# Kernel optimization log

Hardware: AMD Instinct MI355X
Metric: run time of the kernel (lower is better)

The kernel has to match this reference:

```python
import jax, jax.numpy as jnp
import numpy as np
from jax import lax

W = 50      # window size
EPS = 1e-5  # BatchNorm eps (torch default)


def setup_inputs() -> dict:
    key = jax.random.key(0)
    ks = jax.random.split(key, 40)
    def n(i, shape, s=0.1):
        return (jax.random.normal(ks[i], shape, dtype=jnp.float32) * s).astype(jnp.float32)
    inp = {}
    inp['x'] = jax.random.normal(ks[0], (16, 1, 2048), dtype=jnp.float32)
    # conv stack (eval-mode BatchNorm: running mean/var are params)
    inp['conv1_w'] = n(1, (64, 1, 9));  inp['conv1_b'] = n(2, (64,))
    inp['bn1_g'] = 1.0 + n(3, (64,));   inp['bn1_b'] = n(4, (64,))
    inp['bn1_m'] = n(5, (64,));         inp['bn1_v'] = 0.5 + jax.random.uniform(ks[6], (64,), dtype=jnp.float32)
    inp['conv2_w'] = n(7, (32, 64, 7)); inp['conv2_b'] = n(8, (32,))
    inp['bn2_g'] = 1.0 + n(9, (32,));   inp['bn2_b'] = n(10, (32,))
    inp['bn2_m'] = n(11, (32,));        inp['bn2_v'] = 0.5 + jax.random.uniform(ks[12], (32,), dtype=jnp.float32)
    inp['conv3_w'] = n(13, (16, 32, 5)); inp['conv3_b'] = n(14, (16,))
    inp['bn3_g'] = 1.0 + n(15, (16,));   inp['bn3_b'] = n(16, (16,))
    inp['bn3_m'] = n(17, (16,));         inp['bn3_v'] = 0.5 + jax.random.uniform(ks[18], (16,), dtype=jnp.float32)
    # 2-layer LSTM, hidden 64, input 16 (torch gate order i,f,g,o)
    H = 64
    inp['wih0'] = n(19, (4 * H, 16)); inp['whh0'] = n(20, (4 * H, H))
    inp['bih0'] = n(21, (4 * H,));    inp['bhh0'] = n(22, (4 * H,))
    inp['wih1'] = n(23, (4 * H, H));  inp['whh1'] = n(24, (4 * H, H))
    inp['bih1'] = n(25, (4 * H,));    inp['bhh1'] = n(26, (4 * H,))
    # classifier 64 -> 32 -> 2
    inp['fc1_w'] = n(27, (32, H)); inp['fc1_b'] = n(28, (32,))
    inp['fc2_w'] = n(29, (2, 32)); inp['fc2_b'] = n(30, (2,))
    return inp


def _conv1d(x, w, b, pad):
    # x: [N, Cin, L], w: [Cout, Cin, K]
    y = lax.conv_general_dilated(x, w, (1,), [(pad, pad)],
                                 dimension_numbers=('NCH', 'OIH', 'NCH'))
    return y + b[:, None]


def _bn(x, g, b, m, v):
    # eval-mode BatchNorm1d over channel dim of [N, C, L]
    return (x - m[:, None]) * (g / jnp.sqrt(v + EPS))[:, None] + b[:, None]


def _lstm_layer(x, wih, whh, bih, bhh):
    # x: [B, T, D] -> [B, T, H]; torch gate order (i, f, g, o)
    B, T, D = x.shape
    H = whh.shape[1]
    xs = jnp.transpose(x, (1, 0, 2))                     # [T, B, D]
    pre = xs @ wih.T + (bih + bhh)                       # [T, B, 4H] input projection, hoisted
    def step(carry, p):
        h, c = carry
        g = p + h @ whh.T
        i, f, gg, o = jnp.split(g, 4, axis=-1)
        c = jax.nn.sigmoid(f) * c + jax.nn.sigmoid(i) * jnp.tanh(gg)
        h = jax.nn.sigmoid(o) * jnp.tanh(c)
        return (h, c), h
    h0 = jnp.zeros((B, H), x.dtype)
    _, hs = lax.scan(step, (h0, h0), pre)
    return jnp.transpose(hs, (1, 0, 2))


def reference(x, conv1_w, conv1_b, bn1_g, bn1_b, bn1_m, bn1_v,
              conv2_w, conv2_b, bn2_g, bn2_b, bn2_m, bn2_v,
              conv3_w, conv3_b, bn3_g, bn3_b, bn3_m, bn3_v,
              wih0, whh0, bih0, bhh0, wih1, whh1, bih1, bhh1,
              fc1_w, fc1_b, fc2_w, fc2_b):
    B, C, T = x.shape
    # sliding windows with left zero-pad of W-1 -> [B, T, C, W]
    xp = jnp.pad(x, ((0, 0), (0, 0), (W - 1, 0)))
    idx = jnp.arange(T)[:, None] + jnp.arange(W)[None, :]  # [T, W]
    win = xp[:, :, idx]                                    # [B, C, T, W]
    win = jnp.transpose(win, (0, 2, 1, 3)).reshape(B * T, C, W)
    # conv -> BN(eval) -> ReLU stack (dropout is identity in eval)
    h = jax.nn.relu(_bn(_conv1d(win, conv1_w, conv1_b, 4), bn1_g, bn1_b, bn1_m, bn1_v))
    h = jax.nn.relu(_bn(_conv1d(h, conv2_w, conv2_b, 3), bn2_g, bn2_b, bn2_m, bn2_v))
    h = jax.nn.relu(_bn(_conv1d(h, conv3_w, conv3_b, 2), bn3_g, bn3_b, bn3_m, bn3_v))
    feats = h.mean(axis=-1).reshape(B, T, -1)              # AdaptiveAvgPool1d(1) -> [B, T, 16]
    # 2-layer LSTM
    h1 = _lstm_layer(feats, wih0, whh0, bih0, bhh0)
    h2 = _lstm_layer(h1, wih1, whh1, bih1, bhh1)           # [B, T, 64]
    # classifier
    z = jax.nn.relu(h2 @ fc1_w.T + fc1_b)
    logits = z @ fc2_w.T + fc2_b                           # [B, T, 2]
    return logits
```

## Files before the change

### kernel.cpp

```cpp
#include <hip/hip_runtime.h>

#define EPSV 1e-5f
#define SCOPE_AGENT __HIP_MEMORY_SCOPE_AGENT

__device__ __forceinline__ float fast_rcp(float x) { return __builtin_amdgcn_rcpf(x); }
__device__ __forceinline__ float tanhfast(float x) {
    float e = __expf(2.0f * x);
    return 1.0f - 2.0f * fast_rcp(e + 1.0f);
}
__device__ __forceinline__ float dot4(const float4 w, const float4 v, float a) {
    a = fmaf(w.x, v.x, a);
    a = fmaf(w.y, v.y, a);
    a = fmaf(w.z, v.z, a);
    a = fmaf(w.w, v.w, a);
    return a;
}
#define DPPF(v, ctrl) __int_as_float(__builtin_amdgcn_mov_dpp(__float_as_int(v), (ctrl), 0xF, 0xF, false))

typedef unsigned long long ull;

struct CnnS {
    float winh[64];
    float w1t[576];
    float a1[64 * 84 + 32];
    float a2[32 * 56 + 16];
    float s1[64], t1[64], s2[32], t2[32], s3[16], t3[16];
    float psum[256];
};
struct RecS {
    float hbuf[2][80];
    float ring[16][64];
    float xst[16][80];
};

__global__ void pack_kernel(const float* __restrict__ w2, const float* __restrict__ w3,
                            float* __restrict__ w2t2, float4* __restrict__ w3p4,
                            float* __restrict__ w3p1, int* __restrict__ sync_ints) {
    int j = blockIdx.x * 256 + threadIdx.x;
    if (j < 16384) {
        int i = j >> 8;
        int o = (j >> 3) & 31;
        int k = j & 7;
        w2t2[j] = (k < 7) ? w2[o * 448 + i * 7 + k] : 0.0f;
    } else if (j < 16896) {
        int e = j - 16384;
        int i = e >> 4, o = e & 15;
        int base = o * 160 + i * 5;
        w3p4[e] = make_float4(w3[base], w3[base + 1], w3[base + 2], w3[base + 3]);
        w3p1[e] = w3[base + 4];
    } else if (j < 16896 + 4096) {
        sync_ints[j - 16896] = 0;
    }
}

__device__ __forceinline__ void rec0_body(char* smemraw, int b,
    const float* __restrict__ feats,
    const float* __restrict__ wih, const float* __restrict__ whh,
    const float* __restrict__ bih, const float* __restrict__ bhh,
    float* __restrict__ hout, int* __restrict__ cnt0, int* __restrict__ flag1)
{
    RecS* s = (RecS*)smemraw;
    const int tid = threadIdx.x;
    const int j = tid >> 2, kq = tid & 3;

    const float4* pa = (const float4*)(whh + (0 * 64 + j) * 64 + kq * 16);
    const float4* pb = (const float4*)(whh + (1 * 64 + j) * 64 + kq * 16);
    const float4* pc_ = (const float4*)(whh + (2 * 64 + j) * 64 + kq * 16);
    const float4* pd = (const float4*)(whh + (3 * 64 + j) * 64 + kq * 16);
    float4 A0 = pa[0], A1 = pa[1], A2 = pa[2], A3 = pa[3];
    float4 B0 = pb[0], B1 = pb[1], B2 = pb[2], B3 = pb[3];
    float4 C0 = pc_[0], C1 = pc_[1], C2 = pc_[2], C3 = pc_[3];
    float4 D0 = pd[0], D1 = pd[1], D2 = pd[2], D3 = pd[3];
    float4 xw0 = *(const float4*)(wih + (0 * 64 + j) * 16 + kq * 4);
    float4 xw1 = *(const float4*)(wih + (1 * 64 + j) * 16 + kq * 4);
    float4 xw2 = *(const float4*)(wih + (2 * 64 + j) * 16 + kq * 4);
    float4 xw3 = *(const float4*)(wih + (3 * 64 + j) * 16 + kq * 4);
    const float bb0 = bih[j] + bhh[j];
    const float bb1 = bih[64 + j] + bhh[64 + j];
    const float bb2 = bih[128 + j] + bhh[128 + j];
    const float bb3 = bih[192 + j] + bhh[192 + j];

    if (tid < 64) s->hbuf[1][(tid >> 4) * 20 + (tid & 15)] = 0.0f;
    float cst = 0.0f;
    const float* fbase = feats + (long)b * 32768;
    __syncthreads();

#define STEP0(k) { \
        const float4* hp_ = (const float4*)&s->hbuf[((k) + 1) & 1][kq * 20]; \
        float4 h0_ = hp_[0], h1_ = hp_[1], h2_ = hp_[2], h3_ = hp_[3]; \
        float4 xv_ = *(const float4*)&s->xst[(k)][kq * 4]; \
        float p0 = dot4(A3, h3_, dot4(A2, h2_, dot4(A1, h1_, dot4(A0, h0_, dot4(xw0, xv_, 0.f))))); \
        float p1 = dot4(B3, h3_, dot4(B2, h2_, dot4(B1, h1_, dot4(B0, h0_, dot4(xw1, xv_, 0.f))))); \
        float p2 = dot4(C3, h3_, dot4(C2, h2_, dot4(C1, h1_, dot4(C0, h0_, dot4(xw2, xv_, 0.f))))); \
        float p3 = dot4(D3, h3_, dot4(D2, h2_, dot4(D1, h1_, dot4(D0, h0_, dot4(xw3, xv_, 0.f))))); \
        p0 += DPPF(p0, 0xB1); p1 += DPPF(p1, 0xB1); p2 += DPPF(p2, 0xB1); p3 += DPPF(p3, 0xB1); \
        p0 += DPPF(p0, 0x4E); p1 += DPPF(p1, 0x4E); p2 += DPPF(p2, 0x4E); p3 += DPPF(p3, 0x4E); \
        float gi = 1.0f - fast_rcp(__expf(p0 + bb0) + 1.0f); \
        float gf = 1.0f - fast_rcp(__expf(p1 + bb1) + 1.0f); \
        float gg = 1.0f - 2.0f * fast_rcp(__expf(2.0f * (p2 + bb2)) + 1.0f); \
        float go = 1.0f - fast_rcp(__expf(p3 + bb3) + 1.0f); \
        cst = fmaf(gf, cst, gi * gg); \
        float h_ = go * tanhfast(cst); \
        if (kq == 0) { s->hbuf[(k) & 1][(j >> 4) * 20 + (j & 15)] = h_; s->ring[(k)][j] = h_; } \
        __syncthreads(); \
    }

    for (int c = 0; c < 128; ++c) {
        if (tid == 0) {
            while (__hip_atomic_load(&cnt0[b * 128 + c], __ATOMIC_RELAXED, SCOPE_AGENT) < 16)
                __builtin_amdgcn_s_sleep(2);
        }
        __syncthreads();
        s->xst[tid >> 4][tid & 15] =
            __hip_atomic_load(fbase + c * 256 + tid, __ATOMIC_RELAXED, SCOPE_AGENT);
        __syncthreads();
        STEP0(0)  STEP0(1)  STEP0(2)  STEP0(3)
        STEP0(4)  STEP0(5)  STEP0(6)  STEP0(7)
        STEP0(8)  STEP0(9)  STEP0(10) STEP0(11)
        STEP0(12) STEP0(13) STEP0(14) STEP0(15)
        {
            ull* dst = (ull*)(hout + ((long)b * 2048 + c * 16) * 64);
            ull v0 = ((const ull*)s->ring)[tid];
            ull v1 = ((const ull*)s->ring)[tid + 256];
            __hip_atomic_store(dst + tid, v0, __ATOMIC_RELAXED, SCOPE_AGENT);
            __hip_atomic_store(dst + tid + 256, v1, __ATOMIC_RELAXED, SCOPE_AGENT);
            __syncthreads();
            if (tid == 0)
                __hip_atomic_store(&flag1[b * 128 + c], 1, __ATOMIC_RELAXED, SCOPE_AGENT);
        }
    }
#undef STEP0
}

__device__ __forceinline__ void rec1_body(char* smemraw, int b,
    const float* __restrict__ h1o,
    const float* __restrict__ wih, const float* __restrict__ whh,
    const float* __restrict__ bih, const float* __restrict__ bhh,
    float* __restrict__ hout, int* __restrict__ flag1)
{
    RecS* s = (RecS*)smemraw;
    const int tid = threadIdx.x;
    const int j = tid >> 2, kq = tid & 3;

    const float4* pa = (const float4*)(whh + (0 * 64 + j) * 64 + kq * 16);
    const float4* pb = (const float4*)(whh + (1 * 64 + j) * 64 + kq * 16);
    const float4* pc_ = (const float4*)(whh + (2 * 64 + j) * 64 + kq * 16);
    const float4* pd = (const float4*)(whh + (3 * 64 + j) * 64 + kq * 16);
    float4 A0 = pa[0], A1 = pa[1], A2 = pa[2], A3 = pa[3];
    float4 B0 = pb[0], B1 = pb[1], B2 = pb[2], B3 = pb[3];
    float4 C0 = pc_[0], C1 = pc_[1], C2 = pc_[2], C3 = pc_[3];
    float4 D0 = pd[0], D1 = pd[1], D2 = pd[2], D3 = pd[3];
    const float4* qa = (const float4*)(wih + (0 * 64 + j) * 64 + kq * 16);
    const float4* qb = (const float4*)(wih + (1 * 64 + j) * 64 + kq * 16);
    const float4* qc = (const float4*)(wih + (2 * 64 + j) * 64 + kq * 16);
    const float4* qd = (const float4*)(wih + (3 * 64 + j) * 64 + kq * 16);
    float4 XA0 = qa[0], XA1 = qa[1], XA2 = qa[2], XA3 = qa[3];
    float4 XB0 = qb[0], XB1 = qb[1], XB2 = qb[2], XB3 = qb[3];
    float4 XC0 = qc[0], XC1 = qc[1], XC2 = qc[2], XC3 = qc[3];
    float4 XD0 = qd[0], XD1 = qd[1], XD2 = qd[2], XD3 = qd[3];
    const float bb0 = bih[j] + bhh[j];
    const float bb1 = bih[64 + j] + bhh[64 + j];
    const float bb2 = bih[128 + j] + bhh[128 + j];
    const float bb3 = bih[192 + j] + bhh[192 + j];

    if (tid < 64) s->hbuf[1][(tid >> 4) * 20 + (tid & 15)] = 0.0f;
    float cst = 0.0f;
    __syncthreads();

#define STEP1(k) { \
        const float4* hp_ = (const float4*)&s->hbuf[((k) + 1) & 1][kq * 20]; \
        float4 h0_ = hp_[0], h1_ = hp_[1], h2_ = hp_[2], h3_ = hp_[3]; \
        const float4* xp_ = (const float4*)&s->xst[(k)][kq * 20]; \
        float4 x0_ = xp_[0], x1_ = xp_[1], x2_ = xp_[2], x3_ = xp_[3]; \
        float p0 = dot4(A3, h3_, dot4(A2, h2_, dot4(A1, h1_, dot4(A0, h0_, \
                   dot4(XA3, x3_, dot4(XA2, x2_, dot4(XA1, x1_, dot4(XA0, x0_, 0.f)))))))); \
        float p1 = dot4(B3, h3_, dot4(B2, h2_, dot4(B1, h1_, dot4(B0, h0_, \
                   dot4(XB3, x3_, dot4(XB2, x2_, dot4(XB1, x1_, dot4(XB0, x0_, 0.f)))))))); \
        float p2 = dot4(C3, h3_, dot4(C2, h2_, dot4(C1, h1_, dot4(C0, h0_, \
                   dot4(XC3, x3_, dot4(XC2, x2_, dot4(XC1, x1_, dot4(XC0, x0_, 0.f)))))))); \
        float p3 = dot4(D3, h3_, dot4(D2, h2_, dot4(D1, h1_, dot4(D0, h0_, \
                   dot4(XD3, x3_, dot4(XD2, x2_, dot4(XD1, x1_, dot4(XD0, x0_, 0.f)))))))); \
        p0 += DPPF(p0, 0xB1); p1 += DPPF(p1, 0xB1); p2 += DPPF(p2, 0xB1); p3 += DPPF(p3, 0xB1); \
        p0 += DPPF(p0, 0x4E); p1 += DPPF(p1, 0x4E); p2 += DPPF(p2, 0x4E); p3 += DPPF(p3, 0x4E); \
        float gi = 1.0f - fast_rcp(__expf(p0 + bb0) + 1.0f); \
        float gf = 1.0f - fast_rcp(__expf(p1 + bb1) + 1.0f); \
        float gg = 1.0f - 2.0f * fast_rcp(__expf(2.0f * (p2 + bb2)) + 1.0f); \
        float go = 1.0f - fast_rcp(__expf(p3 + bb3) + 1.0f); \
        cst = fmaf(gf, cst, gi * gg); \
        float h_ = go * tanhfast(cst); \
        if (kq == 0) { s->hbuf[(k) & 1][(j >> 4) * 20 + (j & 15)] = h_; s->ring[(k)][j] = h_; } \
        __syncthreads(); \
    }

    for (int c = 0; c < 128; ++c) {
        if (tid == 0) {
            while (__hip_atomic_load(&flag1[b * 128 + c], __ATOMIC_RELAXED, SCOPE_AGENT) < 1)
                __builtin_amdgcn_s_sleep(2);
        }
        __syncthreads();
        {
            const ull* src = (const ull*)(h1o + ((long)b * 2048 + c * 16) * 64);
            ull v0 = __hip_atomic_load(src + tid, __ATOMIC_RELAXED, SCOPE_AGENT);
            ull v1 = __hip_atomic_load(src + tid + 256, __ATOMIC_RELAXED, SCOPE_AGENT);
            int u0 = tid, u1 = tid + 256;
            int k0 = u0 >> 5, p0i = (u0 & 31) * 2;
            int k1 = u1 >> 5, p1i = (u1 & 31) * 2;
            *(ull*)&s->xst[k0][(p0i >> 4) * 20 + (p0i & 15)] = v0;
            *(ull*)&s->xst[k1][(p1i >> 4) * 20 + (p1i & 15)] = v1;
        }
        __syncthreads();
        STEP1(0)  STEP1(1)  STEP1(2)  STEP1(3)
        STEP1(4)  STEP1(5)  STEP1(6)  STEP1(7)
        STEP1(8)  STEP1(9)  STEP1(10) STEP1(11)
        STEP1(12) STEP1(13) STEP1(14) STEP1(15)
        {
            float4* dst = (float4*)(hout + ((long)b * 2048 + c * 16) * 64);
            dst[tid] = ((const float4*)s->ring)[tid];
        }
    }
#undef STEP1
}

__global__ __launch_bounds__(256, 2) void fused_kernel(
    const float* __restrict__ x,
    const float* __restrict__ w1, const float* __restrict__ b1,
    const float* __restrict__ g1, const float* __restrict__ be1,
    const float* __restrict__ m1, const float* __restrict__ v1,
    const float* __restrict__ b2,
    const float* __restrict__ g2, const float* __restrict__ be2,
    const float* __restrict__ m2, const float* __restrict__ v2,
    const float* __restrict__ b3,
    const float* __restrict__ g3, const float* __restrict__ be3,
    const float* __restrict__ m3, const float* __restrict__ v3,
    const float* __restrict__ w2t2,
    const float4* __restrict__ w3p4, const float* __restrict__ w3p1,
    const float* __restrict__ wih0, const float* __restrict__ whh0,
    const float* __restrict__ bih0, const float* __restrict__ bhh0,
    const float* __restrict__ wih1, const float* __restrict__ whh1,
    const float* __restrict__ bih1, const float* __restrict__ bhh1,
    float* __restrict__ feats, float* __restrict__ h1o, float* __restrict__ h2o,
    int* __restrict__ cnt0, int* __restrict__ flag1)
{
    __shared__ __align__(16) char smem[sizeof(CnnS)];
    static_assert(sizeof(RecS) <= sizeof(CnnS), "RecS must fit in CnnS");

    if (blockIdx.x < 16) { rec0_body(smem, blockIdx.x, feats, wih0, whh0, bih0, bhh0, h1o, cnt0, flag1); return; }
    if (blockIdx.x < 32) { rec1_body(smem, blockIdx.x - 16, h1o, wih1, whh1, bih1, bhh1, h2o, flag1); return; }

    CnnS* cs = (CnnS*)smem;
    const int tid = threadIdx.x;
    const int w = blockIdx.x - 32;
    const int b = w & 15;
    const int t = w >> 4;

    for (int idx = tid; idx < 576; idx += 256) {
        int o = idx / 9, k = idx % 9;
        cs->w1t[k * 64 + o] = w1[idx];
    }
    if (tid < 64) {
        float s = g1[tid] * rsqrtf(v1[tid] + EPSV);
        cs->s1[tid] = s;
        cs->t1[tid] = (b1[tid] - m1[tid]) * s + be1[tid];
    } else if (tid < 96) {
        int o = tid - 64;
        float s = g2[o] * rsqrtf(v2[o] + EPSV);
        cs->s2[o] = s;
        cs->t2[o] = (b2[o] - m2[o]) * s + be2[o];
    } else if (tid < 112) {
        int o = tid - 96;
        float s = g3[o] * rsqrtf(v3[o] + EPSV);
        cs->s3[o] = s;
        cs->t3[o] = (b3[o] - m3[o]) * s + be3[o];
    }
    if (tid < 64) {
        cs->winh[tid] = 0.0f;
        float* r = &cs->a1[tid * 84];
        r[0] = 0.f; r[1] = 0.f; r[2] = 0.f;
        r[77] = 0.f; r[78] = 0.f; r[79] = 0.f;
    }
    if (tid < 32) {
        float* r = &cs->a2[tid * 56];
        r[0] = 0.f; r[1] = 0.f;
        r[52] = 0.f; r[53] = 0.f; r[54] = 0.f; r[55] = 0.f;
    }
    __syncthreads();
    if (tid < 50) {
        int gi = t + tid - 49;
        cs->winh[4 + tid] = (gi >= 0) ? x[b * 2048 + gi] : 0.0f;
    }
    __syncthreads();

    {
        int o = tid >> 2, pg = tid & 3;
        int p0 = pg * 13;
        float wv[9];
        #pragma unroll
        for (int k = 0; k < 9; ++k) wv[k] = cs->w1t[k * 64 + o];
        float sc = cs->s1[o], tc = cs->t1[o];
        #pragma unroll
        for (int q = 0; q < 13; ++q) {
            int p = p0 + q;
            if (p < 50) {
                float acc = 0.0f;
                #pragma unroll
                for (int k = 0; k < 9; ++k) acc = fmaf(wv[k], cs->winh[p + k], acc);
                int pi = p + 3;
                int slot = pi + ((pi >> 3) << 2);
                cs->a1[o * 84 + slot] = fmaxf(acc * sc + tc, 0.0f);
            }
        }
    }
    __syncthreads();

    {
        int o = tid >> 3, pg = tid & 7;
        float acc[8];
        #pragma unroll
        for (int q = 0; q < 8; ++q) acc[q] = 0.0f;
        for (int i = 0; i < 64; ++i) {
            const float* rowp = &cs->a1[i * 84 + 12 * pg];
            float4 A0 = *(const float4*)&rowp[0];
            float4 A1 = *(const float4*)&rowp[4];
            float4 A2 = *(const float4*)&rowp[12];
            float2 A3 = *(const float2*)&rowp[16];
            const float4* wp = (const float4*)&w2t2[(i * 32 + o) * 8];
            float4 Wa = wp[0], Wb = wp[1];
            float av[14] = {A0.x, A0.y, A0.z, A0.w, A1.x, A1.y, A1.z, A1.w,
                            A2.x, A2.y, A2.z, A2.w, A3.x, A3.y};
            float wk[7] = {Wa.x, Wa.y, Wa.z, Wa.w, Wb.x, Wb.y, Wb.z};
            #pragma unroll
            for (int k = 0; k < 7; ++k) {
                #pragma unroll
                for (int q = 0; q < 8; ++q) acc[q] = fmaf(wk[k], av[q + k], acc[q]);
            }
        }
        float sc = cs->s2[o], tc = cs->t2[o];
        float r[8];
        #pragma unroll
        for (int q = 0; q < 8; ++q) r[q] = fmaxf(acc[q] * sc + tc, 0.0f);
        float* row = &cs->a2[o * 56 + 8 * pg];
        if (pg < 6) {
            *(float2*)&row[2] = make_float2(r[0], r[1]);
            *(float4*)&row[4] = make_float4(r[2], r[3], r[4], r[5]);
            *(float2*)&row[8] = make_float2(r[6], r[7]);
        } else if (pg == 6) {
            *(float2*)&row[2] = make_float2(r[0], r[1]);
        }
    }
    __syncthreads();

    {
        int o = tid & 15, pg = tid >> 4;
        float acc[4];
        #pragma unroll
        for (int q = 0; q < 4; ++q) acc[q] = 0.0f;
        for (int i = 0; i < 32; ++i) {
            float4 wa = w3p4[i * 16 + o];
            float w4 = w3p1[i * 16 + o];
            const float4* ap = (const float4*)&cs->a2[i * 56 + 4 * pg];
            float4 Aa = ap[0], Ab = ap[1];
            float av[8] = {Aa.x, Aa.y, Aa.z, Aa.w, Ab.x, Ab.y, Ab.z, Ab.w};
            #pragma unroll
            for (int q = 0; q < 4; ++q) {
                acc[q] = fmaf(wa.x, av[q], acc[q]);
                acc[q] = fmaf(wa.y, av[q + 1], acc[q]);
                acc[q] = fmaf(wa.z, av[q + 2], acc[q]);
                acc[q] = fmaf(wa.w, av[q + 3], acc[q]);
                acc[q] = fmaf(w4,   av[q + 4], acc[q]);
            }
        }
        float sc = cs->s3[o], tc = cs->t3[o];
        float ps = 0.0f;
        #pragma unroll
        for (int q = 0; q < 4; ++q) {
            int p = 4 * pg + q;
            if (p < 50) ps += fmaxf(acc[q] * sc + tc, 0.0f);
        }
        cs->psum[pg * 16 + o] = ps;
    }
    __syncthreads();

    if (tid < 16) {
        float s = 0.0f;
        #pragma unroll
        for (int pg = 0; pg < 16; ++pg) s += cs->psum[pg * 16 + tid];
        __hip_atomic_store(&feats[((long)b * 2048 + t) * 16 + tid], s * (1.0f / 50.0f),
                           __ATOMIC_RELAXED, SCOPE_AGENT);
    }
    __syncthreads();
    if (tid == 0)
        __hip_atomic_fetch_add(&cnt0[b * 128 + (t >> 4)], 1, __ATOMIC_RELAXED, SCOPE_AGENT);
}

__global__ __launch_bounds__(256) void fc_kernel(
    const float* __restrict__ h2o,
    const float* __restrict__ fc1w, const float* __restrict__ fc1b,
    const float* __restrict__ fc2w, const float* __restrict__ fc2b,
    float* __restrict__ out)
{
    int r = blockIdx.x * 256 + threadIdx.x;
    float h[64];
    const float4* hp = (const float4*)(h2o + (long)r * 64);
    #pragma unroll
    for (int i = 0; i < 16; ++i) {
        float4 v = hp[i];
        h[4 * i] = v.x; h[4 * i + 1] = v.y; h[4 * i + 2] = v.z; h[4 * i + 3] = v.w;
    }
    float l0 = fc2b[0], l1 = fc2b[1];
    #pragma unroll 4
    for (int j = 0; j < 32; ++j) {
        float z = fc1b[j];
        #pragma unroll
        for (int k = 0; k < 64; ++k) z = fmaf(h[k], fc1w[j * 64 + k], z);
        z = fmaxf(z, 0.0f);
        l0 = fmaf(z, fc2w[j], l0);
        l1 = fmaf(z, fc2w[32 + j], l1);
    }
    out[r * 2] = l0;
    out[r * 2 + 1] = l1;
}

extern "C" void kernel_launch(void* const* d_in, const int* in_sizes, int n_in,
                              void* d_out, int out_size, void* d_ws, size_t ws_size,
                              hipStream_t stream) {
    const float* x    = (const float*)d_in[0];
    const float* w1   = (const float*)d_in[1];
    const float* b1   = (const float*)d_in[2];
    const float* g1   = (const float*)d_in[3];
    const float* be1  = (const float*)d_in[4];
    const float* m1   = (const float*)d_in[5];
    const float* v1   = (const float*)d_in[6];
    const float* w2   = (const float*)d_in[7];
    const float* b2   = (const float*)d_in[8];
    const float* g2   = (const float*)d_in[9];
    const float* be2  = (const float*)d_in[10];
    const float* m2   = (const float*)d_in[11];
    const float* v2   = (const float*)d_in[12];
    const float* w3   = (const float*)d_in[13];
    const float* b3   = (const float*)d_in[14];
    const float* g3   = (const float*)d_in[15];
    const float* be3  = (const float*)d_in[16];
    const float* m3   = (const float*)d_in[17];
    const float* v3   = (const float*)d_in[18];
    const float* wih0 = (const float*)d_in[19];
    const float* whh0 = (const float*)d_in[20];
    const float* bih0 = (const float*)d_in[21];
    const float* bhh0 = (const float*)d_in[22];
    const float* wih1 = (const float*)d_in[23];
    const float* whh1 = (const float*)d_in[24];
    const float* bih1 = (const float*)d_in[25];
    const float* bhh1 = (const float*)d_in[26];
    const float* fc1w = (const float*)d_in[27];
    const float* fc1b = (const float*)d_in[28];
    const float* fc2w = (const float*)d_in[29];
    const float* fc2b = (const float*)d_in[30];
    float* out = (float*)d_out;

    float* ws    = (float*)d_ws;
    float* feats = ws;
    float* h2o   = feats + 32768 * 16;
    float* w2t2  = h2o + 32768 * 64;
    float* w3p4f = w2t2 + 16384;
    float* w3p1  = w3p4f + 2048;
    float* h1o   = w3p1 + 512;
    int*   cnt0  = (int*)(h1o + 32768 * 64);
    int*   flag1 = cnt0 + 2048;

    hipLaunchKernelGGL(pack_kernel, dim3(82), dim3(256), 0, stream,
                       w2, w3, w2t2, (float4*)w3p4f, w3p1, cnt0);
    hipLaunchKernelGGL(fused_kernel, dim3(32 + 32768), dim3(256), 0, stream,
                       x, w1, b1, g1, be1, m1, v1, b2, g2, be2, m2, v2,
                       b3, g3, be3, m3, v3, w2t2, (const float4*)w3p4f, w3p1,
                       wih0, whh0, bih0, bhh0, wih1, whh1, bih1, bhh1,
                       feats, h1o, h2o, cnt0, flag1);
    hipLaunchKernelGGL(fc_kernel, dim3(128), dim3(256), 0, stream,
                       h2o, fc1w, fc1b, fc2w, fc2b, out);
}
```

Before: 1.339 ms.

## Share interior conv outputs across overlapping windows; compute only edge positions per window

```diff
diff --git a/kernel.cpp b/kernel.cpp
--- a/kernel.cpp
+++ b/kernel.cpp
@@ -19,18 +19,18 @@
 
 typedef unsigned long long ull;
 
-struct CnnS {
-    float winh[64];
-    float w1t[576];
-    float a1[64 * 84 + 32];
-    float a2[32 * 56 + 16];
-    float s1[64], t1[64], s2[32], t2[32], s3[16], t3[16];
-    float psum[256];
-};
 struct RecS {
     float hbuf[2][80];
     float ring[16][64];
     float xst[16][80];
+};
+struct EdgeS {
+    float A1[64 * 40];
+    float A2[32 * 32];
+    float xeL[24], xeR[24];
+    float s1[64], t1[64], s2[32], t2[32], s3[16], t3[16];
+    float psumE[288];
+    float pi[512];
 };
 
 __global__ void pack_kernel(const float* __restrict__ w2, const float* __restrict__ w3,
@@ -50,6 +50,147 @@
         w3p1[e] = w3[base + 4];
     } else if (j < 16896 + 4096) {
         sync_ints[j - 16896] = 0;
+    }
+}
+
+__global__ __launch_bounds__(256) void conv1f_kernel(
+    const float* __restrict__ x, const float* __restrict__ w1,
+    const float* __restrict__ b1, const float* __restrict__ g1,
+    const float* __restrict__ be1, const float* __restrict__ m1,
+    const float* __restrict__ vv1, float* __restrict__ a1f)
+{
+    __shared__ float xs[72];
+    const int tid = threadIdx.x;
+    const int T = blockIdx.x * 64;
+    const int b = blockIdx.y;
+    if (tid < 72) {
+        int gi = T - 49 + tid;
+        xs[tid] = (gi >= 0 && gi < 2048) ? x[b * 2048 + gi] : 0.0f;
+    }
+    const int i = tid & 63, q = tid >> 6;
+    float wv[9];
+    #pragma unroll
+    for (int k = 0; k < 9; ++k) wv[k] = w1[i * 9 + k];
+    float sc = g1[i] * rsqrtf(vv1[i] + EPSV);
+    float tc = (b1[i] - m1[i]) * sc + be1[i];
+    __syncthreads();
+    #pragma unroll
+    for (int r = 0; r < 16; ++r) {
+        int v1 = T + q * 16 + r;
+        if (v1 < 2089) {
+            float acc = 0.0f;
+            #pragma unroll
+            for (int k = 0; k < 9; ++k) acc = fmaf(wv[k], xs[q * 16 + r + k], acc);
+            a1f[((long)b * 2089 + v1) * 64 + i] = fmaxf(acc * sc + tc, 0.0f);
+        }
+    }
+}
+
+__global__ __launch_bounds__(256) void conv2f_kernel(
+    const float* __restrict__ a1f, const float* __restrict__ w2t2,
+    const float* __restrict__ b2, const float* __restrict__ g2,
+    const float* __restrict__ be2, const float* __restrict__ m2,
+    const float* __restrict__ vv2, float* __restrict__ a2f)
+{
+    __shared__ __align__(16) float As[64 * 104];
+    const int tid = threadIdx.x;
+    const int T = blockIdx.x * 64;
+    const int b = blockIdx.y;
+    for (int idx = tid; idx < 1120; idx += 256) {
+        int j = idx >> 4, i4 = (idx & 15) * 4;
+        int v1 = T + j; if (v1 > 2088) v1 = 2088;
+        float4 f = *(const float4*)&a1f[((long)b * 2089 + v1) * 64 + i4];
+        int sj = j + ((j >> 3) << 2);
+        As[(i4 + 0) * 104 + sj] = f.x;
+        As[(i4 + 1) * 104 + sj] = f.y;
+        As[(i4 + 2) * 104 + sj] = f.z;
+        As[(i4 + 3) * 104 + sj] = f.w;
+    }
+    const int o = tid >> 3, pg = tid & 7;
+    float sc = g2[o] * rsqrtf(vv2[o] + EPSV);
+    float tc = (b2[o] - m2[o]) * sc + be2[o];
+    __syncthreads();
+    float acc[8];
+    #pragma unroll
+    for (int q = 0; q < 8; ++q) acc[q] = 0.0f;
+    for (int i = 0; i < 64; ++i) {
+        const float* rowp = &As[i * 104 + 12 * pg];
+        float4 A0 = *(const float4*)&rowp[0];
+        float4 A1 = *(const float4*)&rowp[4];
+        float4 A2 = *(const float4*)&rowp[12];
+        float2 A3 = *(const float2*)&rowp[16];
+        const float4* wp = (const float4*)&w2t2[(i * 32 + o) * 8];
+        float4 Wa = wp[0], Wb = wp[1];
+        float av[14] = {A0.x, A0.y, A0.z, A0.w, A1.x, A1.y, A1.z, A1.w,
+                        A2.x, A2.y, A2.z, A2.w, A3.x, A3.y};
+        float wk[7] = {Wa.x, Wa.y, Wa.z, Wa.w, Wb.x, Wb.y, Wb.z};
+        #pragma unroll
+        for (int k = 0; k < 7; ++k) {
+            #pragma unroll
+            for (int q = 0; q < 8; ++q) acc[q] = fmaf(wk[k], av[q + k], acc[q]);
+        }
+    }
+    #pragma unroll
+    for (int q = 0; q < 8; ++q) {
+        int v2 = T + pg * 8 + q;
+        if (v2 < 2083)
+            a2f[((long)b * 2083 + v2) * 32 + o] = fmaxf(acc[q] * sc + tc, 0.0f);
+    }
+}
+
+__global__ __launch_bounds__(256) void conv3f_kernel(
+    const float* __restrict__ a2f,
+    const float4* __restrict__ w3p4, const float* __restrict__ w3p1,
+    const float* __restrict__ b3, const float* __restrict__ g3,
+    const float* __restrict__ be3, const float* __restrict__ m3,
+    const float* __restrict__ vv3, float* __restrict__ a3f)
+{
+    __shared__ __align__(16) float A2s[32 * 200];
+    const int tid = threadIdx.x;
+    const int T = blockIdx.x * 128;
+    const int b = blockIdx.y;
+    for (int idx = tid; idx < 1056; idx += 256) {
+        int j = idx >> 3, i4 = (idx & 7) * 4;
+        int v2 = T + j; if (v2 > 2082) v2 = 2082;
+        float4 f = *(const float4*)&a2f[((long)b * 2083 + v2) * 32 + i4];
+        int sj = j + ((j >> 3) << 2);
+        A2s[(i4 + 0) * 200 + sj] = f.x;
+        A2s[(i4 + 1) * 200 + sj] = f.y;
+        A2s[(i4 + 2) * 200 + sj] = f.z;
+        A2s[(i4 + 3) * 200 + sj] = f.w;
+    }
+    const int o = tid & 15, pg = tid >> 4;
+    float sc = g3[o] * rsqrtf(vv3[o] + EPSV);
+    float tc = (b3[o] - m3[o]) * sc + be3[o];
+    __syncthreads();
+    float acc[8];
+    #pragma unroll
+    for (int q = 0; q < 8; ++q) acc[q] = 0.0f;
+    for (int i = 0; i < 32; ++i) {
+        const float* rowp = &A2s[i * 200 + 12 * pg];
+        float4 R0 = *(const float4*)&rowp[0];
+        float4 R1 = *(const float4*)&rowp[4];
+        float4 R2 = *(const float4*)&rowp[12];
+        float av[12] = {R0.x, R0.y, R0.z, R0.w, R1.x, R1.y, R1.z, R1.w,
+                        R2.x, R2.y, R2.z, R2.w};
+        float4 wa = w3p4[i * 16 + o];
+        float w4 = w3p1[i * 16 + o];
+        #pragma unroll
+        for (int q = 0; q < 8; ++q) {
+            acc[q] = fmaf(wa.x, av[q], acc[q]);
+            acc[q] = fmaf(wa.y, av[q + 1], acc[q]);
+            acc[q] = fmaf(wa.z, av[q + 2], acc[q]);
+            acc[q] = fmaf(wa.w, av[q + 3], acc[q]);
+            acc[q] = fmaf(w4,   av[q + 4], acc[q]);
+        }
+    }
+    #pragma unroll
+    for (int q = 0; q < 8; ++q) {
+        int v3 = T + pg * 8 + q;
+        if (v3 < 2079)
+            a3f[((long)b * 2080 + v3) * 16 + o] = fmaxf(acc[q] * sc + tc, 0.0f);
+        else if (v3 < 2080)
+            a3f[((long)b * 2080 + v3) * 16 + o] = 0.0f;
     }
 }
 
@@ -221,19 +362,173 @@
 #undef STEP1
 }
 
+__device__ __forceinline__ void edge_body(char* smemraw, int b, int t,
+    const float* __restrict__ x,
+    const float* __restrict__ w1,
+    const float* __restrict__ b1, const float* __restrict__ g1,
+    const float* __restrict__ be1, const float* __restrict__ m1, const float* __restrict__ vv1,
+    const float* __restrict__ b2, const float* __restrict__ g2,
+    const float* __restrict__ be2, const float* __restrict__ m2, const float* __restrict__ vv2,
+    const float* __restrict__ b3, const float* __restrict__ g3,
+    const float* __restrict__ be3, const float* __restrict__ m3, const float* __restrict__ vv3,
+    const float* __restrict__ w2t2,
+    const float4* __restrict__ w3p4, const float* __restrict__ w3p1,
+    const float* __restrict__ a3f,
+    float* __restrict__ feats, int* __restrict__ cnt0)
+{
+    EdgeS* s = (EdgeS*)smemraw;
+    const int tid = threadIdx.x;
+
+    if (tid < 128) {
+        int dv = tid >> 2, o4 = (tid & 3) * 4;
+        *(float4*)&s->pi[dv * 16 + o4] =
+            *(const float4*)&a3f[((long)b * 2080 + t + dv) * 16 + o4];
+    }
+    if (tid < 64) {
+        float sc = g1[tid] * rsqrtf(vv1[tid] + EPSV);
+        s->s1[tid] = sc;
+        s->t1[tid] = (b1[tid] - m1[tid]) * sc + be1[tid];
+    } else if (tid < 96) {
+        int o = tid - 64;
+        float sc = g2[o] * rsqrtf(vv2[o] + EPSV);
+        s->s2[o] = sc;
+        s->t2[o] = (b2[o] - m2[o]) * sc + be2[o];
+    } else if (tid < 112) {
+        int o = tid - 96;
+        float sc = g3[o] * rsqrtf(vv3[o] + EPSV);
+        s->s3[o] = sc;
+        s->t3[o] = (b3[o] - m3[o]) * sc + be3[o];
+    } else if (tid < 136) {
+        int j = tid - 112;
+        float v = 0.0f;
+        if (j >= 4 && j < 22) { int gi = t - 53 + j; if (gi >= 0) v = x[b * 2048 + gi]; }
+        s->xeL[j] = v;
+    } else if (tid < 160) {
+        int j = tid - 136;
+        float v = 0.0f;
+        if (j <= 17) { int gi = t - 17 + j; if (gi >= 0) v = x[b * 2048 + gi]; }
+        s->xeR[j] = v;
+    }
+    for (int idx = tid; idx < 384; idx += 256) {
+        int o = idx / 6, z = idx - o * 6;
+        s->A1[o * 40 + (z < 3 ? z : 31 + z)] = 0.0f;
+    }
+    if (tid < 128) {
+        int o = tid >> 2, z = tid & 3;
+        s->A2[o * 32 + (z < 2 ? z : 25 + z)] = 0.0f;
+    }
+    __syncthreads();
+
+    {
+        int o = tid >> 2, g = tid & 3;
+        float wv[9];
+        #pragma unroll
+        for (int k = 0; k < 9; ++k) wv[k] = w1[o * 9 + k];
+        float sc = s->s1[o], tc = s->t1[o];
+        #pragma unroll
+        for (int n = 0; n < 7; ++n) {
+            int P = g * 7 + n;
+            float acc = 0.0f;
+            if (P < 14) {
+                #pragma unroll
+                for (int k = 0; k < 9; ++k) acc = fmaf(wv[k], s->xeL[P + k], acc);
+                s->A1[o * 40 + 3 + P] = fmaxf(acc * sc + tc, 0.0f);
+            } else {
+                int pr = P - 14;
+                #pragma unroll
+                for (int k = 0; k < 9; ++k) acc = fmaf(wv[k], s->xeR[pr + k], acc);
+                s->A1[o * 40 + 20 + pr] = fmaxf(acc * sc + tc, 0.0f);
+            }
+        }
+    }
+    __syncthreads();
+
+    {
+        int o = tid >> 3, g = tid & 7;
+        int side = g >> 2, gg = g & 3;
+        int be_ = gg * 3;
+        int cnt = (gg == 3) ? 2 : 3;
+        int beta0 = side ? 20 + be_ : be_;
+        float acc0 = 0.f, acc1 = 0.f, acc2 = 0.f;
+        for (int i = 0; i < 64; ++i) {
+            const float* rp = &s->A1[i * 40 + beta0];
+            float av[9];
+            #pragma unroll
+            for (int c = 0; c < 9; ++c) av[c] = rp[c];
+            const float4* wp = (const float4*)&w2t2[(i * 32 + o) * 8];
+            float4 Wa = wp[0], Wb = wp[1];
+            float wk[7] = {Wa.x, Wa.y, Wa.z, Wa.w, Wb.x, Wb.y, Wb.z};
+            #pragma unroll
+            for (int k = 0; k < 7; ++k) {
+                acc0 = fmaf(wk[k], av[k], acc0);
+                acc1 = fmaf(wk[k], av[k + 1], acc1);
+                acc2 = fmaf(wk[k], av[k + 2], acc2);
+            }
+        }
+        float sc = s->s2[o], tc = s->t2[o];
+        float r0 = fmaxf(acc0 * sc + tc, 0.0f);
+        float r1 = fmaxf(acc1 * sc + tc, 0.0f);
+        float r2 = fmaxf(acc2 * sc + tc, 0.0f);
+        int base = o * 32 + (side ? 16 + be_ : 2 + be_);
+        s->A2[base] = r0;
+        s->A2[base + 1] = r1;
+        if (cnt == 3) s->A2[base + 2] = r2;
+    }
+    __syncthreads();
+
+    {
+        int o = tid & 15, g = tid >> 4;
+        float sc = s->s3[o], tc = s->t3[o];
+        #pragma unroll
+        for (int rep = 0; rep < 2; ++rep) {
+            int P3 = (rep == 0) ? g : 16 + g;
+            if (rep == 1 && g >= 2) break;
+            int tb = (P3 >= 9) ? 16 + (P3 - 9) : P3;
+            float acc = 0.0f;
+            for (int i = 0; i < 32; ++i) {
+                const float* rp = &s->A2[i * 32 + tb];
+                float4 wa = w3p4[i * 16 + o];
+                float w4 = w3p1[i * 16 + o];
+                acc = fmaf(wa.x, rp[0], acc);
+                acc = fmaf(wa.y, rp[1], acc);
+                acc = fmaf(wa.z, rp[2], acc);
+                acc = fmaf(wa.w, rp[3], acc);
+                acc = fmaf(w4,   rp[4], acc);
+            }
+            s->psumE[P3 * 16 + o] = fmaxf(acc * sc + tc, 0.0f);
+        }
+    }
+    __syncthreads();
+
+    if (tid < 16) {
+        float e = 0.0f;
+        #pragma unroll
+        for (int P3 = 0; P3 < 18; ++P3) e += s->psumE[P3 * 16 + tid];
+        float ii = 0.0f;
+        #pragma unroll
+        for (int dv = 0; dv < 32; ++dv) ii += s->pi[dv * 16 + tid];
+        __hip_atomic_store(&feats[((long)b * 2048 + t) * 16 + tid], (e + ii) * (1.0f / 50.0f),
+                           __ATOMIC_RELAXED, SCOPE_AGENT);
+    }
+    __syncthreads();
+    if (tid == 0)
+        __hip_atomic_fetch_add(&cnt0[b * 128 + (t >> 4)], 1, __ATOMIC_RELAXED, SCOPE_AGENT);
+}
+
 __global__ __launch_bounds__(256, 2) void fused_kernel(
     const float* __restrict__ x,
     const float* __restrict__ w1, const float* __restrict__ b1,
     const float* __restrict__ g1, const float* __restrict__ be1,
-    const float* __restrict__ m1, const float* __restrict__ v1,
+    const float* __restrict__ m1, const float* __restrict__ vv1,
     const float* __restrict__ b2,
     const float* __restrict__ g2, const float* __restrict__ be2,
-    const float* __restrict__ m2, const float* __restrict__ v2,
+    const float* __restrict__ m2, const float* __restrict__ vv2,
     const float* __restrict__ b3,
     const float* __restrict__ g3, const float* __restrict__ be3,
-    const float* __restrict__ m3, const float* __restrict__ v3,
+    const float* __restrict__ m3, const float* __restrict__ vv3,
     const float* __restrict__ w2t2,
     const float4* __restrict__ w3p4, const float* __restrict__ w3p1,
+    const float* __restrict__ a3f,
     const float* __restrict__ wih0, const float* __restrict__ whh0,
     const float* __restrict__ bih0, const float* __restrict__ bhh0,
     const float* __restrict__ wih1, const float* __restrict__ whh1,
@@ -241,155 +536,16 @@
     float* __restrict__ feats, float* __restrict__ h1o, float* __restrict__ h2o,
     int* __restrict__ cnt0, int* __restrict__ flag1)
 {
-    __shared__ __align__(16) char smem[sizeof(CnnS)];
-    static_assert(sizeof(RecS) <= sizeof(CnnS), "RecS must fit in CnnS");
+    __shared__ __align__(16) char smem[sizeof(EdgeS) > sizeof(RecS) ? sizeof(EdgeS) : sizeof(RecS)];
 
     if (blockIdx.x < 16) { rec0_body(smem, blockIdx.x, feats, wih0, whh0, bih0, bhh0, h1o, cnt0, flag1); return; }
     if (blockIdx.x < 32) { rec1_body(smem, blockIdx.x - 16, h1o, wih1, whh1, bih1, bhh1, h2o, flag1); return; }
 
-    CnnS* cs = (CnnS*)smem;
-    const int tid = threadIdx.x;
-    const int w = blockIdx.x - 32;
-    const int b = w & 15;
-    const int t = w >> 4;
-
-    for (int idx = tid; idx < 576; idx += 256) {
-        int o = idx / 9, k = idx % 9;
-        cs->w1t[k * 64 + o] = w1[idx];
-    }
-    if (tid < 64) {
-        float s = g1[tid] * rsqrtf(v1[tid] + EPSV);
-        cs->s1[tid] = s;
-        cs->t1[tid] = (b1[tid] - m1[tid]) * s + be1[tid];
-    } else if (tid < 96) {
-        int o = tid - 64;
-        float s = g2[o] * rsqrtf(v2[o] + EPSV);
-        cs->s2[o] = s;
-        cs->t2[o] = (b2[o] - m2[o]) * s + be2[o];
-    } else if (tid < 112) {
-        int o = tid - 96;
-        float s = g3[o] * rsqrtf(v3[o] + EPSV);
-        cs->s3[o] = s;
-        cs->t3[o] = (b3[o] - m3[o]) * s + be3[o];
-    }
-    if (tid < 64) {
-        cs->winh[tid] = 0.0f;
-        float* r = &cs->a1[tid * 84];
-        r[0] = 0.f; r[1] = 0.f; r[2] = 0.f;
-        r[77] = 0.f; r[78] = 0.f; r[79] = 0.f;
-    }
-    if (tid < 32) {
-        float* r = &cs->a2[tid * 56];
-        r[0] = 0.f; r[1] = 0.f;
-        r[52] = 0.f; r[53] = 0.f; r[54] = 0.f; r[55] = 0.f;
-    }
-    __syncthreads();
-    if (tid < 50) {
-        int gi = t + tid - 49;
-        cs->winh[4 + tid] = (gi >= 0) ? x[b * 2048 + gi] : 0.0f;
-    }
-    __syncthreads();
-
-    {
-        int o = tid >> 2, pg = tid & 3;
-        int p0 = pg * 13;
-        float wv[9];
-        #pragma unroll
-        for (int k = 0; k < 9; ++k) wv[k] = cs->w1t[k * 64 + o];
-        float sc = cs->s1[o], tc = cs->t1[o];
-        #pragma unroll
-        for (int q = 0; q < 13; ++q) {
-            int p = p0 + q;
-            if (p < 50) {
-                float acc = 0.0f;
-                #pragma unroll
-                for (int k = 0; k < 9; ++k) acc = fmaf(wv[k], cs->winh[p + k], acc);
-                int pi = p + 3;
-                int slot = pi + ((pi >> 3) << 2);
-                cs->a1[o * 84 + slot] = fmaxf(acc * sc + tc, 0.0f);
-            }
-        }
-    }
-    __syncthreads();
-
-    {
-        int o = tid >> 3, pg = tid & 7;
-        float acc[8];
-        #pragma unroll
-        for (int q = 0; q < 8; ++q) acc[q] = 0.0f;
-        for (int i = 0; i < 64; ++i) {
-            const float* rowp = &cs->a1[i * 84 + 12 * pg];
-            float4 A0 = *(const float4*)&rowp[0];
-            float4 A1 = *(const float4*)&rowp[4];
-            float4 A2 = *(const float4*)&rowp[12];
-            float2 A3 = *(const float2*)&rowp[16];
-            const float4* wp = (const float4*)&w2t2[(i * 32 + o) * 8];
-            float4 Wa = wp[0], Wb = wp[1];
-            float av[14] = {A0.x, A0.y, A0.z, A0.w, A1.x, A1.y, A1.z, A1.w,
-                            A2.x, A2.y, A2.z, A2.w, A3.x, A3.y};
-            float wk[7] = {Wa.x, Wa.y, Wa.z, Wa.w, Wb.x, Wb.y, Wb.z};
-            #pragma unroll
-            for (int k = 0; k < 7; ++k) {
-                #pragma unroll
-                for (int q = 0; q < 8; ++q) acc[q] = fmaf(wk[k], av[q + k], acc[q]);
-            }
-        }
-        float sc = cs->s2[o], tc = cs->t2[o];
-        float r[8];
-        #pragma unroll
-        for (int q = 0; q < 8; ++q) r[q] = fmaxf(acc[q] * sc + tc, 0.0f);
-        float* row = &cs->a2[o * 56 + 8 * pg];
-        if (pg < 6) {
-            *(float2*)&row[2] = make_float2(r[0], r[1]);
-            *(float4*)&row[4] = make_float4(r[2], r[3], r[4], r[5]);
-            *(float2*)&row[8] = make_float2(r[6], r[7]);
-        } else if (pg == 6) {
-            *(float2*)&row[2] = make_float2(r[0], r[1]);
-        }
-    }
-    __syncthreads();
-
-    {
-        int o = tid & 15, pg = tid >> 4;
-        float acc[4];
-        #pragma unroll
-        for (int q = 0; q < 4; ++q) acc[q] = 0.0f;
-        for (int i = 0; i < 32; ++i) {
-            float4 wa = w3p4[i * 16 + o];
-            float w4 = w3p1[i * 16 + o];
-            const float4* ap = (const float4*)&cs->a2[i * 56 + 4 * pg];
-            float4 Aa = ap[0], Ab = ap[1];
-            float av[8] = {Aa.x, Aa.y, Aa.z, Aa.w, Ab.x, Ab.y, Ab.z, Ab.w};
-            #pragma unroll
-            for (int q = 0; q < 4; ++q) {
-                acc[q] = fmaf(wa.x, av[q], acc[q]);
-                acc[q] = fmaf(wa.y, av[q + 1], acc[q]);
-                acc[q] = fmaf(wa.z, av[q + 2], acc[q]);
-                acc[q] = fmaf(wa.w, av[q + 3], acc[q]);
-                acc[q] = fmaf(w4,   av[q + 4], acc[q]);
-            }
-        }
-        float sc = cs->s3[o], tc = cs->t3[o];
-        float ps = 0.0f;
-        #pragma unroll
-        for (int q = 0; q < 4; ++q) {
-            int p = 4 * pg + q;
-            if (p < 50) ps += fmaxf(acc[q] * sc + tc, 0.0f);
-        }
-        cs->psum[pg * 16 + o] = ps;
-    }
-    __syncthreads();
-
-    if (tid < 16) {
-        float s = 0.0f;
-        #pragma unroll
-        for (int pg = 0; pg < 16; ++pg) s += cs->psum[pg * 16 + tid];
-        __hip_atomic_store(&feats[((long)b * 2048 + t) * 16 + tid], s * (1.0f / 50.0f),
-                           __ATOMIC_RELAXED, SCOPE_AGENT);
-    }
-    __syncthreads();
-    if (tid == 0)
-        __hip_atomic_fetch_add(&cnt0[b * 128 + (t >> 4)], 1, __ATOMIC_RELAXED, SCOPE_AGENT);
+    int w = blockIdx.x - 32;
+    int b = w & 15;
+    int t = w >> 4;
+    edge_body(smem, b, t, x, w1, b1, g1, be1, m1, vv1, b2, g2, be2, m2, vv2,
+              b3, g3, be3, m3, vv3, w2t2, w3p4, w3p1, a3f, feats, cnt0);
 }
 
 __global__ __launch_bounds__(256) void fc_kernel(
@@ -463,14 +619,23 @@
     float* w3p4f = w2t2 + 16384;
     float* w3p1  = w3p4f + 2048;
     float* h1o   = w3p1 + 512;
-    int*   cnt0  = (int*)(h1o + 32768 * 64);
+    float* a1f   = h1o + 32768 * 64;
+    float* a2f   = a1f + 16 * 2089 * 64;
+    float* a3f   = a2f + 16 * 2083 * 32;
+    int*   cnt0  = (int*)(a3f + 16 * 2080 * 16);
     int*   flag1 = cnt0 + 2048;
 
     hipLaunchKernelGGL(pack_kernel, dim3(82), dim3(256), 0, stream,
                        w2, w3, w2t2, (float4*)w3p4f, w3p1, cnt0);
+    hipLaunchKernelGGL(conv1f_kernel, dim3(33, 16), dim3(256), 0, stream,
+                       x, w1, b1, g1, be1, m1, v1, a1f);
+    hipLaunchKernelGGL(conv2f_kernel, dim3(33, 16), dim3(256), 0, stream,
+                       a1f, w2t2, b2, g2, be2, m2, v2, a2f);
+    hipLaunchKernelGGL(conv3f_kernel, dim3(17, 16), dim3(256), 0, stream,
+                       a2f, (const float4*)w3p4f, w3p1, b3, g3, be3, m3, v3, a3f);
     hipLaunchKernelGGL(fused_kernel, dim3(32 + 32768), dim3(256), 0, stream,
                        x, w1, b1, g1, be1, m1, v1, b2, g2, be2, m2, v2,
-                       b3, g3, be3, m3, v3, w2t2, (const float4*)w3p4f, w3p1,
+                       b3, g3, be3, m3, v3, w2t2, (const float4*)w3p4f, w3p1, a3f,
                        wih0, whh0, bih0, bhh0, wih1, whh1, bih1, bhh1,
                        feats, h1o, h2o, cnt0, flag1);
     hipLaunchKernelGGL(fc_kernel, dim3(128), dim3(256), 0, stream,
```

Result: faster. 1.198 ms (-10.6%).
